# Kernel optimization log

Measured on AMD Instinct MI355X. Metric: run time of the kernel, lower is better.

Reference implementation:

```python
import jax, jax.numpy as jnp
import numpy as np

B, L, DC, DD, A = 32, 1024, 1024, 1024, 1024
NEG = -1e10


def setup_inputs() -> dict:
    key = jax.random.key(0)
    ks = jax.random.split(key, 16)
    s = lambda fan_in: 1.0 / np.sqrt(fan_in)
    return {
        "caption_features": jax.random.normal(ks[0], (B, L, DC), jnp.float32),
        "decoder_hidden": jax.random.normal(ks[1], (B, DD), jnp.float32),
        "word": jax.random.normal(ks[2], (B, DC), jnp.float32),
        "prev_caption_mask": jax.random.randint(ks[3], (B, L), 0, 2, jnp.int32),
        # cap_features_att: Linear(DC, A)
        "Wf": jax.random.uniform(ks[4], (A, DC), jnp.float32, -s(DC), s(DC)),
        "bf": jax.random.uniform(ks[5], (A,), jnp.float32, -s(DC), s(DC)),
        # cap_decoder_att: Linear(DD, A)
        "Wd": jax.random.uniform(ks[6], (A, DD), jnp.float32, -s(DD), s(DD)),
        "bd": jax.random.uniform(ks[7], (A,), jnp.float32, -s(DD), s(DD)),
        # cap_full_att: Linear(A, 1)
        "Wa": jax.random.uniform(ks[8], (1, A), jnp.float32, -s(A), s(A)),
        "ba": jax.random.uniform(ks[9], (1,), jnp.float32, -s(A), s(A)),
        # context_gate: Linear(2*DC + DD, DC)
        "Wg": jax.random.uniform(ks[10], (DC, 2 * DC + DD), jnp.float32, -s(2 * DC + DD), s(2 * DC + DD)),
        "bg": jax.random.uniform(ks[11], (DC,), jnp.float32, -s(2 * DC + DD), s(2 * DC + DD)),
        # sc_affine: Linear(DC, DC)
        "Ws": jax.random.uniform(ks[12], (DC, DC), jnp.float32, -s(DC), s(DC)),
        "bs": jax.random.uniform(ks[13], (DC,), jnp.float32, -s(DC), s(DC)),
        # tc_affine: Linear(2*DD, DC)
        "Wt": jax.random.uniform(ks[14], (DC, 2 * DD), jnp.float32, -s(2 * DD), s(2 * DD)),
        "bt": jax.random.uniform(ks[15], (DC,), jnp.float32, -s(2 * DD), s(2 * DD)),
    }


def reference(caption_features, decoder_hidden, word, prev_caption_mask,
              Wf, bf, Wd, bd, Wa, ba, Wg, bg, Ws, bs, Wt, bt):
    # additive (Bahdanau) attention scores: (B, L)
    att1 = jnp.einsum('bld,ad->bla', caption_features, Wf) + bf          # (B, L, A)
    att2 = decoder_hidden @ Wd.T + bd                                    # (B, A)
    scores = jnp.einsum('bla,a->bl', jnp.tanh(att1 + att2[:, None, :]), Wa[0]) + ba[0]
    scores = jnp.where(prev_caption_mask == 0, NEG, scores)
    alpha = jax.nn.softmax(scores, axis=1)                               # (B, L)
    context = jnp.einsum('bl,bld->bd', alpha, caption_features)          # (B, DC)
    # gated fusion
    zt = jax.nn.sigmoid(jnp.concatenate([word, decoder_hidden, context], axis=1) @ Wg.T + bg)
    sc = jnp.tanh(context @ Ws.T + bs)
    tc = jnp.tanh(jnp.concatenate([word, decoder_hidden], axis=1) @ Wt.T + bt)
    gated_context = zt * sc + (1.0 - zt) * tc
    return (gated_context, alpha)
```

## Files before the change

### kernel.cpp

```cpp
#include <hip/hip_runtime.h>
#include <hip/hip_bf16.h>
#include <cstdint>
#include <cstddef>

#define LOG2E 1.4426950408889634f

typedef __attribute__((ext_vector_type(8))) short short8;
typedef __attribute__((ext_vector_type(4))) float f32x4;

__device__ __forceinline__ float exp2f_fast(float x) { return __builtin_amdgcn_exp2f(x); }
__device__ __forceinline__ float rcp_fast(float x)   { return __builtin_amdgcn_rcpf(x); }
__device__ __forceinline__ float tanh_fast(float x) {
  float e = exp2f_fast(x * (2.0f * LOG2E));
  return 1.0f - 2.0f * rcp_fast(e + 1.0f);
}
__device__ __forceinline__ unsigned short f2b(float f) {
  union { float f; unsigned int u; } v; v.f = f;
  return (unsigned short)((v.u + 0x7FFFu + ((v.u >> 16) & 1u)) >> 16);
}
__device__ __forceinline__ float b2f(short h) {
  union { unsigned u; float f; } w; w.u = ((unsigned)(unsigned short)h) << 16;
  return w.f;
}

#define GLOAD_LDS16(g, l) \
  __builtin_amdgcn_global_load_lds((const __attribute__((address_space(1))) unsigned int*)(g), \
                                   (__attribute__((address_space(3))) unsigned int*)(l), 16, 0, 0)

__device__ __forceinline__ void skinny_gemm(
    const float* __restrict__ W, int Kfull,
    const float* __restrict__ x0, const float* __restrict__ x1,
    const float* __restrict__ x2,
    int kbeg, int kend, int n0, float* __restrict__ out)
{
  __shared__ unsigned char sX[4096];
  const int tid = threadIdx.x, lane = tid & 63, wv = tid >> 6;
  const int l15 = lane & 15, l4 = lane >> 4;
  f32x4 acc[2][2];
#pragma unroll
  for (int m = 0; m < 2; ++m)
#pragma unroll
    for (int j = 0; j < 2; ++j) acc[m][j] = (f32x4){0.f, 0.f, 0.f, 0.f};

  const int srow = tid >> 3, skc = (tid & 7) * 8;
  const int sbyte = srow * 128 + ((skc * 2) ^ ((srow & 7) << 4));

  for (int k0 = kbeg; k0 < kend; k0 += 64) {
    const float* xs = (k0 < 1024) ? x0 : (k0 < 2048) ? x1 : x2;
    const float* xp = xs + srow * 1024 + (k0 & 1023) + skc;
    float4 a = *reinterpret_cast<const float4*>(xp);
    float4 b = *reinterpret_cast<const float4*>(xp + 4);
    short8 h;
    h[0] = (short)f2b(a.x); h[1] = (short)f2b(a.y); h[2] = (short)f2b(a.z); h[3] = (short)f2b(a.w);
    h[4] = (short)f2b(b.x); h[5] = (short)f2b(b.y); h[6] = (short)f2b(b.z); h[7] = (short)f2b(b.w);
    *reinterpret_cast<short8*>(sX + sbyte) = h;
    __syncthreads();
#pragma unroll
    for (int ks = 0; ks < 2; ++ks) {
      short8 af[2], bfr[2];
#pragma unroll
      for (int m = 0; m < 2; ++m) {
        int r = m * 16 + l15;
        af[m] = *reinterpret_cast<const short8*>(
            sX + r * 128 + (((ks * 64) + l4 * 16) ^ ((r & 7) << 4)));
      }
#pragma unroll
      for (int j = 0; j < 2; ++j) {
        int n = n0 + wv * 32 + j * 16 + l15;
        const float* wp = W + (size_t)n * Kfull + k0 + ks * 32 + l4 * 8;
        float4 wa = *reinterpret_cast<const float4*>(wp);
        float4 wb = *reinterpret_cast<const float4*>(wp + 4);
        short8 hb;
        hb[0] = (short)f2b(wa.x); hb[1] = (short)f2b(wa.y); hb[2] = (short)f2b(wa.z); hb[3] = (short)f2b(wa.w);
        hb[4] = (short)f2b(wb.x); hb[5] = (short)f2b(wb.y); hb[6] = (short)f2b(wb.z); hb[7] = (short)f2b(wb.w);
        bfr[j] = hb;
      }
#pragma unroll
      for (int m = 0; m < 2; ++m)
#pragma unroll
        for (int j = 0; j < 2; ++j)
          acc[m][j] = __builtin_amdgcn_mfma_f32_16x16x32_bf16(af[m], bfr[j], acc[m][j], 0, 0, 0);
    }
    __syncthreads();
  }
#pragma unroll
  for (int m = 0; m < 2; ++m)
#pragma unroll
    for (int j = 0; j < 2; ++j)
#pragma unroll
      for (int r = 0; r < 4; ++r)
        atomicAdd(out + (size_t)(m * 16 + l4 * 4 + r) * 1024 + (n0 + wv * 32 + j * 16 + l15),
                  acc[m][j][r]);
}

__global__ __launch_bounds__(256) void convert_att2(
    const float* __restrict__ wf, unsigned short* __restrict__ wfb,
    const float* __restrict__ Wd, const float* __restrict__ dh,
    float* __restrict__ att2, const float* __restrict__ Wg,
    const float* __restrict__ Wt, const float* __restrict__ word,
    float* __restrict__ ztp, float* __restrict__ tcp)
{
  const int bid = blockIdx.x;
  if (bid < 128) {
    const int base = bid * 1024;
#pragma unroll
    for (int j = 0; j < 4; ++j) {
      int g = base + j * 256 + (int)threadIdx.x;
      const float* s = wf + (size_t)g * 8;
      float4 a = *reinterpret_cast<const float4*>(s);
      float4 b = *reinterpret_cast<const float4*>(s + 4);
      short8 o;
      o[0] = (short)f2b(a.x); o[1] = (short)f2b(a.y); o[2] = (short)f2b(a.z); o[3] = (short)f2b(a.w);
      o[4] = (short)f2b(b.x); o[5] = (short)f2b(b.y); o[6] = (short)f2b(b.z); o[7] = (short)f2b(b.w);
      *reinterpret_cast<short8*>(wfb + (size_t)g * 8) = o;
    }
  } else if (bid < 144) {
    int bid2 = bid - 128;
    int nt = bid2 & 7, ks = bid2 >> 3;
    skinny_gemm(Wd, 1024, dh, dh, dh, ks * 512, ks * 512 + 512, nt * 128, att2);
  } else {
    int eb = bid - 144;
    int es = eb >> 3, nt = eb & 7;
    if (es < 4)
      skinny_gemm(Wg, 3072, word, dh, dh, es * 512, es * 512 + 512, nt * 128, ztp);
    else
      skinny_gemm(Wt, 2048, word, dh, dh, (es - 4) * 512, (es - 4) * 512 + 512, nt * 128, tcp);
  }
}

__global__ __launch_bounds__(256) void gate_gemm(
    const float* __restrict__ Wg, const float* __restrict__ Ws_,
    const float* __restrict__ word, const float* __restrict__ dh,
    const float* __restrict__ ctx,
    float* __restrict__ ztp, float* __restrict__ scp)
{
  const int nt = blockIdx.x, slot = blockIdx.y;
  if (slot < 2)
    skinny_gemm(Wg, 3072, word, dh, ctx, 2048 + slot * 512, 2048 + slot * 512 + 512, nt * 128, ztp);
  else
    skinny_gemm(Ws_, 1024, ctx, ctx, ctx, (slot - 2) * 512, (slot - 2) * 512 + 512, nt * 128, scp);
}

__global__ __launch_bounds__(512, 2) void att_gemm3(
    const float* __restrict__ cap, const unsigned short* __restrict__ wfb,
    const float* __restrict__ att2pre, const float* __restrict__ bfv,
    const float* __restrict__ bdv, const float* __restrict__ Wa,
    float* __restrict__ scores)
{
  __shared__ __align__(16) unsigned char lds[131072];
  const int tid = threadIdx.x, lane = tid & 63, wv = tid >> 6;
  const int j = ((int)blockIdx.x & 7) * 64 + ((int)blockIdx.x >> 3);
  const int mt = j >> 2, nt = j & 3;
  const int m0 = mt << 8, n0 = nt << 8;
  const int bb = m0 >> 10;
  const int wm = wv >> 2, wn = wv & 3;
  const int l15 = lane & 15, l4 = lane >> 4;
  const int r8 = lane >> 3, c8 = lane & 7;
  const unsigned swb = (unsigned)((l15 & 7) << 4);

  const float* capA = cap + (size_t)(m0 + wv * 32 + r8) * 1024 +
                      ((unsigned)((c8 * 16) ^ (r8 << 4)) >> 1);
  const unsigned char* bSrc = (const unsigned char*)wfb +
      (size_t)(n0 + wv * 32 + r8) * 2048 + ((c8 * 16) ^ (r8 << 4));
  const unsigned ldsBase = (unsigned)(size_t)(&lds[0]);

  f32x4 acc[8][4];
#pragma unroll
  for (int mf = 0; mf < 8; ++mf)
#pragma unroll
    for (int nf = 0; nf < 4; ++nf) acc[mf][nf] = (f32x4){0.f, 0.f, 0.f, 0.f};

#define STAGE_B(t) do { \
    const int sl__ = (t) & 1; \
    unsigned char* db__ = lds + sl__ * 65536 + 32768 + wv * 4096; \
    const unsigned char* gb__ = bSrc + (t) * 128; \
    GLOAD_LDS16(gb__,          db__); \
    GLOAD_LDS16(gb__ + 16384,  db__ + 1024); \
    GLOAD_LDS16(gb__ + 32768,  db__ + 2048); \
    GLOAD_LDS16(gb__ + 49152,  db__ + 3072); \
  } while (0)

#define FLIGHT(fA0, fA1, fB0, fB1, j0, tt) do { \
    const float* p0__ = capA + (size_t)(j0) * 8192 + (tt) * 64; \
    const float* p1__ = p0__ + 8192; \
    fA0 = *reinterpret_cast<const float4*>(p0__); \
    fA1 = *reinterpret_cast<const float4*>(p0__ + 4); \
    fB0 = *reinterpret_cast<const float4*>(p1__); \
    fB1 = *reinterpret_cast<const float4*>(p1__ + 4); \
  } while (0)

#define PACK_WRITE(fA, fB, wp) do { \
    short8 o__; \
    o__[0] = (short)f2b(fA.x); o__[1] = (short)f2b(fA.y); \
    o__[2] = (short)f2b(fA.z); o__[3] = (short)f2b(fA.w); \
    o__[4] = (short)f2b(fB.x); o__[5] = (short)f2b(fB.y); \
    o__[6] = (short)f2b(fB.z); o__[7] = (short)f2b(fB.w); \
    *reinterpret_cast<short8*>(wp) = o__; \
  } while (0)

#define DSREAD(dst, addr) \
  asm volatile("ds_read_b128 %0, %1" : "=v"(dst) : "v"(addr))

#define READ_AQ(dst, q) do { \
_Pragma("unroll") \
    for (int mf2 = 0; mf2 < 2; ++mf2) \
_Pragma("unroll") \
      for (int ks = 0; ks < 2; ++ks) { \
        unsigned r__ = (unsigned)(wm * 128 + (q) * 32 + mf2 * 16 + l15); \
        DSREAD(dst[mf2 * 2 + ks], sA + r__ * 128 + (((unsigned)(ks * 64 + l4 * 16)) ^ swb)); \
      } \
  } while (0)

#define READ_B(ch) do { \
_Pragma("unroll") \
    for (int nf = 0; nf < 2; ++nf) \
_Pragma("unroll") \
      for (int ks = 0; ks < 2; ++ks) { \
        unsigned c__ = (unsigned)(wn * 64 + (ch) * 32 + nf * 16 + l15); \
        DSREAD(Breg[(ch) * 4 + nf * 2 + ks], sB + c__ * 128 + (((unsigned)(ks * 64 + l4 * 16)) ^ swb)); \
      } \
  } while (0)

#define MFMA8(q, ch, Aq) do { \
    __builtin_amdgcn_s_setprio(1); \
_Pragma("unroll") \
    for (int mf2 = 0; mf2 < 2; ++mf2) \
_Pragma("unroll") \
      for (int nf = 0; nf < 2; ++nf) \
_Pragma("unroll") \
        for (int ks = 0; ks < 2; ++ks) \
          acc[(q) * 2 + mf2][(ch) * 2 + nf] = __builtin_amdgcn_mfma_f32_16x16x32_bf16( \
              Aq[mf2 * 2 + ks], Breg[(ch) * 4 + nf * 2 + ks], acc[(q) * 2 + mf2][(ch) * 2 + nf], 0, 0, 0); \
    __builtin_amdgcn_s_setprio(0); \
  } while (0)

#define WAIT_LGKM(n) do { \
    asm volatile("s_waitcnt lgkmcnt(" #n ")" ::: "memory"); \
    __builtin_amdgcn_sched_barrier(0); \
  } while (0)

  short8 Aq0[4], Aq1[4], Breg[8];
  float4 g0a, g0b, g1a, g1b;
  float4 g2a, g2b, g3a, g3b;

  STAGE_B(0);
  FLIGHT(g0a, g0b, g1a, g1b, 0, 0);
  FLIGHT(g2a, g2b, g3a, g3b, 2, 0);
  asm volatile("s_waitcnt vmcnt(0)" ::: "memory");
  {
    unsigned char* wp = lds + wv * 4096 + lane * 16;
    PACK_WRITE(g0a, g0b, wp);
    PACK_WRITE(g1a, g1b, wp + 1024);
    PACK_WRITE(g2a, g2b, wp + 2048);
    PACK_WRITE(g3a, g3b, wp + 3072);
  }
  FLIGHT(g0a, g0b, g1a, g1b, 0, 1);
  FLIGHT(g2a, g2b, g3a, g3b, 2, 1);
  WAIT_LGKM(0);
  asm volatile("s_barrier" ::: "memory");

  for (int t = 0; t < 16; ++t) {
    const unsigned sA = ldsBase + (unsigned)((t & 1) * 65536);
    const unsigned sB = sA + 32768u;

    if (t < 15) {
      asm volatile("s_waitcnt vmcnt(0)" ::: "memory");
      __builtin_amdgcn_sched_barrier(0);
      unsigned char* wp = lds + ((t + 1) & 1) * 65536 + wv * 4096 + lane * 16;
      PACK_WRITE(g0a, g0b, wp);
      PACK_WRITE(g1a, g1b, wp + 1024);
      PACK_WRITE(g2a, g2b, wp + 2048);
      PACK_WRITE(g3a, g3b, wp + 3072);
    }
    if (t < 15) STAGE_B(t + 1);

    READ_AQ(Aq0, 0);
    READ_B(0);
    READ_B(1);
    READ_AQ(Aq1, 1);

    WAIT_LGKM(8);
    MFMA8(0, 0, Aq0);
    WAIT_LGKM(4);
    MFMA8(0, 1, Aq0);
    WAIT_LGKM(0);
    READ_AQ(Aq0, 2);
    MFMA8(1, 0, Aq1);
    MFMA8(1, 1, Aq1);
    READ_AQ(Aq1, 3);
    WAIT_LGKM(4);
    MFMA8(2, 0, Aq0);
    MFMA8(2, 1, Aq0);
    if (t < 14) FLIGHT(g0a, g0b, g1a, g1b, 0, t + 2);
    WAIT_LGKM(0);
    MFMA8(3, 0, Aq1);
    MFMA8(3, 1, Aq1);
    if (t < 14) FLIGHT(g2a, g2b, g3a, g3b, 2, t + 2);

    if (t < 15) {
      if (t < 14) {
        asm volatile("s_waitcnt vmcnt(8)" ::: "memory");
      } else {
        asm volatile("s_waitcnt vmcnt(0)" ::: "memory");
      }
      asm volatile("s_barrier" ::: "memory");
    }
  }

  float colb[4], wav[4];
#pragma unroll
  for (int nf = 0; nf < 4; ++nf) {
    int cg = n0 + wn * 64 + nf * 16 + l15;
    colb[nf] = att2pre[bb * 1024 + cg] + bfv[cg] + bdv[cg];
    wav[nf]  = Wa[cg];
  }
#pragma unroll
  for (int mf = 0; mf < 8; ++mf) {
#pragma unroll
    for (int r = 0; r < 4; ++r) {
      float s = tanh_fast(acc[mf][0][r] + colb[0]) * wav[0]
              + tanh_fast(acc[mf][1][r] + colb[1]) * wav[1]
              + tanh_fast(acc[mf][2][r] + colb[2]) * wav[2]
              + tanh_fast(acc[mf][3][r] + colb[3]) * wav[3];
      s += __shfl_xor(s, 1);
      s += __shfl_xor(s, 2);
      s += __shfl_xor(s, 4);
      s += __shfl_xor(s, 8);
      if (l15 == 0)
        atomicAdd(scores + (m0 + wm * 128 + mf * 16 + l4 * 4 + r), s);
    }
  }
#undef STAGE_B
#undef FLIGHT
#undef PACK_WRITE
#undef DSREAD
#undef READ_AQ
#undef READ_B
#undef MFMA8
#undef WAIT_LGKM
}

__global__ __launch_bounds__(256) void softmax_k(
    const float* __restrict__ scores, const int* __restrict__ mask,
    float* __restrict__ alpha)
{
  const int b = blockIdx.x, tid = threadIdx.x;
  __shared__ float red[8];
  float s[4];
  float mx = -3.0e38f;
#pragma unroll
  for (int i = 0; i < 4; ++i) {
    int l = tid + i * 256;
    float v = scores[b * 1024 + l];
    v = (mask[b * 1024 + l] == 0) ? -1.0e10f : v;
    s[i] = v;
    mx = fmaxf(mx, v);
  }
  for (int off = 1; off < 64; off <<= 1) mx = fmaxf(mx, __shfl_xor(mx, off));
  int wv = tid >> 6;
  if ((tid & 63) == 0) red[wv] = mx;
  __syncthreads();
  mx = fmaxf(fmaxf(red[0], red[1]), fmaxf(red[2], red[3]));
  float sum = 0.f;
#pragma unroll
  for (int i = 0; i < 4; ++i) {
    s[i] = exp2f_fast((s[i] - mx) * LOG2E);
    sum += s[i];
  }
  for (int off = 1; off < 64; off <<= 1) sum += __shfl_xor(sum, off);
  if ((tid & 63) == 0) red[4 + wv] = sum;
  __syncthreads();
  sum = red[4] + red[5] + red[6] + red[7];
  float inv = 1.0f / sum;
#pragma unroll
  for (int i = 0; i < 4; ++i) alpha[b * 1024 + tid + i * 256] = s[i] * inv;
}

__global__ __launch_bounds__(256) void ctx_kb(
    const float* __restrict__ cap, const float* __restrict__ alpha,
    float* __restrict__ ctx)
{
  const int b = blockIdx.y, lc = blockIdx.x;
  const int dc = threadIdx.x & 127, loff = threadIdx.x >> 7;
  float acc[8] = {0.f, 0.f, 0.f, 0.f, 0.f, 0.f, 0.f, 0.f};
  for (int l = lc * 128 + loff; l < lc * 128 + 128; l += 2) {
    float av = alpha[b * 1024 + l];
    if (av != 0.f) {
      const float* p = cap + (((size_t)(b * 1024 + l)) << 10) + dc * 8;
      float4 v0 = *reinterpret_cast<const float4*>(p);
      float4 v1 = *reinterpret_cast<const float4*>(p + 4);
      acc[0] += av * v0.x; acc[1] += av * v0.y;
      acc[2] += av * v0.z; acc[3] += av * v0.w;
      acc[4] += av * v1.x; acc[5] += av * v1.y;
      acc[6] += av * v1.z; acc[7] += av * v1.w;
    }
  }
#pragma unroll
  for (int j = 0; j < 8; ++j) atomicAdd(ctx + b * 1024 + dc * 8 + j, acc[j]);
}

__global__ __launch_bounds__(256) void final_k(
    const float* __restrict__ ztp, const float* __restrict__ scp,
    const float* __restrict__ tcp, const float* __restrict__ bg,
    const float* __restrict__ bs, const float* __restrict__ bt,
    float* __restrict__ out)
{
  const int idx = blockIdx.x * 256 + threadIdx.x;
  const int d = idx & 1023;
  float z  = rcp_fast(1.0f + exp2f_fast(-(ztp[idx] + bg[d]) * LOG2E));
  float sc = tanh_fast(scp[idx] + bs[d]);
  float tc = tanh_fast(tcp[idx] + bt[d]);
  out[idx] = z * sc + (1.0f - z) * tc;
}

extern "C" void kernel_launch(void* const* d_in, const int* in_sizes, int n_in,
                              void* d_out, int out_size, void* d_ws, size_t ws_size,
                              hipStream_t stream) {
  const float* cap  = (const float*)d_in[0];
  const float* dh   = (const float*)d_in[1];
  const float* word = (const float*)d_in[2];
  const int*   mask = (const int*)d_in[3];
  const float* Wf   = (const float*)d_in[4];
  const float* bf   = (const float*)d_in[5];
  const float* Wd   = (const float*)d_in[6];
  const float* bd   = (const float*)d_in[7];
  const float* Wa   = (const float*)d_in[8];
  const float* Wg   = (const float*)d_in[10];
  const float* bg   = (const float*)d_in[11];
  const float* Ws   = (const float*)d_in[12];
  const float* bs   = (const float*)d_in[13];
  const float* Wt   = (const float*)d_in[14];
  const float* bt   = (const float*)d_in[15];

  float* out_g = (float*)d_out;
  float* alpha = (float*)d_out + 32768;

  float* att2pre = (float*)d_ws;
  float* scores  = att2pre + 32768;
  float* ctx     = scores + 32768;
  float* ztp     = ctx + 32768;
  float* scp     = ztp + 32768;
  float* tcp     = scp + 32768;
  unsigned short* wfb = (unsigned short*)((char*)d_ws + 786432);

  hipMemsetAsync(d_ws, 0, 6 * 32768 * sizeof(float), stream);

  convert_att2<<<208, 256, 0, stream>>>(Wf, wfb, Wd, dh, att2pre,
                                        Wg, Wt, word, ztp, tcp);
  att_gemm3<<<512, 512, 0, stream>>>(cap, wfb, att2pre, bf, bd, Wa, scores);
  softmax_k<<<32, 256, 0, stream>>>(scores, mask, alpha);
  ctx_kb<<<dim3(8, 32), 256, 0, stream>>>(cap, alpha, ctx);
  gate_gemm<<<dim3(8, 4), 256, 0, stream>>>(Wg, Ws, word, dh, ctx, ztp, scp);
  final_k<<<128, 256, 0, stream>>>(ztp, scp, tcp, bg, bs, bt, out_g);
}
```

Baseline: 156.2 us.

## Restructure GEMM main loop into barrier-separated four-phase MFMA schedule

```diff
diff --git a/kernel.cpp b/kernel.cpp
--- a/kernel.cpp
+++ b/kernel.cpp
@@ -201,36 +201,36 @@
 #define DSREAD(dst, addr) \
   asm volatile("ds_read_b128 %0, %1" : "=v"(dst) : "v"(addr))
 
-#define READ_AQ(dst, q) do { \
-_Pragma("unroll") \
-    for (int mf2 = 0; mf2 < 2; ++mf2) \
+#define READ_A(rh) do { \
+_Pragma("unroll") \
+    for (int mf = 0; mf < 4; ++mf) \
 _Pragma("unroll") \
       for (int ks = 0; ks < 2; ++ks) { \
-        unsigned r__ = (unsigned)(wm * 128 + (q) * 32 + mf2 * 16 + l15); \
-        DSREAD(dst[mf2 * 2 + ks], sA + r__ * 128 + (((unsigned)(ks * 64 + l4 * 16)) ^ swb)); \
+        unsigned r__ = (unsigned)(wm * 128 + (rh) * 64 + mf * 16 + l15); \
+        DSREAD(Areg[mf * 2 + ks], sA + r__ * 128 + (((unsigned)(ks * 64 + l4 * 16)) ^ swb)); \
       } \
   } while (0)
 
-#define READ_B(ch) do { \
+#define READ_B(Breg, ch) do { \
 _Pragma("unroll") \
     for (int nf = 0; nf < 2; ++nf) \
 _Pragma("unroll") \
       for (int ks = 0; ks < 2; ++ks) { \
         unsigned c__ = (unsigned)(wn * 64 + (ch) * 32 + nf * 16 + l15); \
-        DSREAD(Breg[(ch) * 4 + nf * 2 + ks], sB + c__ * 128 + (((unsigned)(ks * 64 + l4 * 16)) ^ swb)); \
+        DSREAD(Breg[nf * 2 + ks], sB + c__ * 128 + (((unsigned)(ks * 64 + l4 * 16)) ^ swb)); \
       } \
   } while (0)
 
-#define MFMA8(q, ch, Aq) do { \
+#define MFMA16(rh, ch, Breg) do { \
     __builtin_amdgcn_s_setprio(1); \
 _Pragma("unroll") \
-    for (int mf2 = 0; mf2 < 2; ++mf2) \
+    for (int mf = 0; mf < 4; ++mf) \
 _Pragma("unroll") \
       for (int nf = 0; nf < 2; ++nf) \
 _Pragma("unroll") \
         for (int ks = 0; ks < 2; ++ks) \
-          acc[(q) * 2 + mf2][(ch) * 2 + nf] = __builtin_amdgcn_mfma_f32_16x16x32_bf16( \
-              Aq[mf2 * 2 + ks], Breg[(ch) * 4 + nf * 2 + ks], acc[(q) * 2 + mf2][(ch) * 2 + nf], 0, 0, 0); \
+          acc[(rh) * 4 + mf][(ch) * 2 + nf] = __builtin_amdgcn_mfma_f32_16x16x32_bf16( \
+              Areg[mf * 2 + ks], Breg[nf * 2 + ks], acc[(rh) * 4 + mf][(ch) * 2 + nf], 0, 0, 0); \
     __builtin_amdgcn_s_setprio(0); \
   } while (0)
 
@@ -239,7 +239,9 @@
     __builtin_amdgcn_sched_barrier(0); \
   } while (0)
 
-  short8 Aq0[4], Aq1[4], Breg[8];
+#define BAR() asm volatile("s_barrier" ::: "memory")
+
+  short8 Areg[8], B0reg[4], B1reg[4];
   float4 g0a, g0b, g1a, g1b;
   float4 g2a, g2b, g3a, g3b;
 
@@ -257,12 +259,20 @@
   FLIGHT(g0a, g0b, g1a, g1b, 0, 1);
   FLIGHT(g2a, g2b, g3a, g3b, 2, 1);
   WAIT_LGKM(0);
-  asm volatile("s_barrier" ::: "memory");
+  BAR();
 
   for (int t = 0; t < 16; ++t) {
     const unsigned sA = ldsBase + (unsigned)((t & 1) * 65536);
     const unsigned sB = sA + 32768u;
 
+    READ_A(0);
+    READ_B(B0reg, 0);
+    BAR();
+    WAIT_LGKM(0);
+    MFMA16(0, 0, B0reg);
+    BAR();
+
+    READ_B(B1reg, 1);
     if (t < 15) {
       asm volatile("s_waitcnt vmcnt(0)" ::: "memory");
       __builtin_amdgcn_sched_barrier(0);
@@ -271,40 +281,33 @@
       PACK_WRITE(g1a, g1b, wp + 1024);
       PACK_WRITE(g2a, g2b, wp + 2048);
       PACK_WRITE(g3a, g3b, wp + 3072);
-    }
-    if (t < 15) STAGE_B(t + 1);
-
-    READ_AQ(Aq0, 0);
-    READ_B(0);
-    READ_B(1);
-    READ_AQ(Aq1, 1);
-
-    WAIT_LGKM(8);
-    MFMA8(0, 0, Aq0);
-    WAIT_LGKM(4);
-    MFMA8(0, 1, Aq0);
+      STAGE_B(t + 1);
+    }
+    BAR();
+    if (t < 15) { WAIT_LGKM(4); }
+    else        { WAIT_LGKM(0); }
+    MFMA16(0, 1, B1reg);
+    BAR();
+
+    READ_A(1);
+    if (t < 14) FLIGHT(g0a, g0b, g1a, g1b, 0, t + 2);
+    BAR();
     WAIT_LGKM(0);
-    READ_AQ(Aq0, 2);
-    MFMA8(1, 0, Aq1);
-    MFMA8(1, 1, Aq1);
-    READ_AQ(Aq1, 3);
-    WAIT_LGKM(4);
-    MFMA8(2, 0, Aq0);
-    MFMA8(2, 1, Aq0);
-    if (t < 14) FLIGHT(g0a, g0b, g1a, g1b, 0, t + 2);
-    WAIT_LGKM(0);
-    MFMA8(3, 0, Aq1);
-    MFMA8(3, 1, Aq1);
+    MFMA16(1, 0, B0reg);
+    BAR();
+
     if (t < 14) FLIGHT(g2a, g2b, g3a, g3b, 2, t + 2);
-
     if (t < 15) {
       if (t < 14) {
         asm volatile("s_waitcnt vmcnt(8)" ::: "memory");
       } else {
         asm volatile("s_waitcnt vmcnt(0)" ::: "memory");
       }
-      asm volatile("s_barrier" ::: "memory");
-    }
+      __builtin_amdgcn_sched_barrier(0);
+    }
+    BAR();
+    MFMA16(1, 1, B1reg);
+    if (t < 15) BAR();
   }
 
   float colb[4], wav[4];
@@ -334,10 +337,11 @@
 #undef FLIGHT
 #undef PACK_WRITE
 #undef DSREAD
-#undef READ_AQ
+#undef READ_A
 #undef READ_B
-#undef MFMA8
+#undef MFMA16
 #undef WAIT_LGKM
+#undef BAR
 }
 
 __global__ __launch_bounds__(256) void softmax_k(
```

Result: slower. 167.6 us (+7.3%).
